# Optimization experiments

Hardware: AMD Instinct MI355X
Metric: run time of the kernel (lower is better)

Reference implementation:

```python
import jax, jax.numpy as jnp
import numpy as np

D, HID = 768, 192          # embed_dim, BiAttention hid_dim (= D//4)
B, LQ, NC, NE = 8, 64, 2048, 1200
NCON, NREL = 100000, 41    # concept vocab, relations (+1 pad)
SCALE = 0.02


def setup_inputs() -> dict:
    key = jax.random.key(0)
    ks = jax.random.split(key, 20)
    n = lambda k, s, sc=SCALE: jax.random.normal(k, s, jnp.float32) * sc
    return {
        'q_hidden_states': jax.random.normal(ks[0], (B, LQ, D), jnp.float32),
        'q_attention_mask': jnp.ones((B, LQ), jnp.bool_),
        'head_cids': jax.random.randint(ks[1], (B, NC), 0, NCON, jnp.int32),
        'distances': jax.random.randint(ks[2], (B, NC), 0, 4, jnp.int32),
        'head_idxs': jax.random.randint(ks[3], (B, NE), 0, NC, jnp.int32),
        'tail_idxs': jax.random.randint(ks[4], (B, NE), 0, NC, jnp.int32),
        'rel_ids': jax.random.randint(ks[5], (B, NE), 0, NREL, jnp.int32),
        'concept_table': n(ks[6], (NCON, D)),
        'dist_table': n(ks[7], (4, D)),
        'rel_table': n(ks[8], (NREL, D)),
        'W_ce': n(ks[9], (2 * D, D)), 'b_ce': jnp.zeros((D,), jnp.float32),
        'W_cs': n(ks[10], (D, 2 * D)), 'b_cs': jnp.zeros((2 * D,), jnp.float32),
        'W_ts': n(ks[11], (D, 5 * D)), 'b_ts': jnp.zeros((5 * D,), jnp.float32),
        'w_in1': n(ks[12], (D,)), 'w_mem1': n(ks[13], (D,)),
        'W_in2': n(ks[14], (D, HID)), 'b_in2': jnp.zeros((HID,), jnp.float32),
        'W_mem2': n(ks[15], (D, HID)), 'b_mem2': jnp.zeros((HID,), jnp.float32),
    }


def biattention(inp, mem, mask, w_in1, w_mem1, W_in2, b_in2, W_mem2, b_mem2):
    # inp: [B,Ld,D], mem: [B,Lm,D], mask: [B,Lm] float. Eval mode -> dropout off.
    input_dot = jnp.einsum('bnd,d->bn', inp, w_in1)[..., None]        # [B,Ld,1]
    memory_dot = jnp.einsum('bld,d->bl', mem, w_mem1)[:, None, :]     # [B,1,Lm]
    cross = jnp.einsum('bnd,bld->bnl', inp, mem) / np.sqrt(D)         # [B,Ld,Lm]
    att = input_dot + memory_dot + cross - 1e30 * (1.0 - mask[:, None, :])
    inp2 = inp @ W_in2 + b_in2                                        # [B,Ld,H]
    mem2 = mem @ W_mem2 + b_mem2                                      # [B,Lm,H]
    w1 = jax.nn.softmax(att, axis=-1)
    out1 = jnp.einsum('bnl,blh->bnh', w1, mem2)
    w2 = jax.nn.softmax(jnp.max(att, axis=-1), axis=-1)               # [B,Ld]
    out2 = jnp.einsum('bn,bnh->bh', w2, inp2)[:, None, :]             # [B,1,H]
    return jnp.concatenate([inp2, out1, inp2 * out1, out2 * out1], axis=-1)


def reference(q_hidden_states, q_attention_mask, head_cids, distances,
              head_idxs, tail_idxs, rel_ids, concept_table, dist_table,
              rel_table, W_ce, b_ce, W_cs, b_cs, W_ts, b_ts,
              w_in1, w_mem1, W_in2, b_in2, W_mem2, b_mem2):
    mask_f = q_attention_mask.astype(jnp.float32)
    # max-pooled question embedding (masked as in torch source)
    q_emb = jnp.max(q_hidden_states * mask_f[:, :, None], axis=1)     # [B,D]
    # concept encoding: gather concept + distance embeddings, fuse with linear
    c_emb = concept_table[head_cids]                                  # [B,NC,D]
    d_emb = dist_table[distances]                                     # [B,NC,D]
    cf = jnp.concatenate([c_emb, d_emb], axis=-1) @ W_ce + b_ce       # [B,NC,D]
    # BiAttention fusion of concepts against question tokens
    fused = biattention(cf, q_hidden_states, mask_f,
                        w_in1, w_mem1, W_in2, b_in2, W_mem2, b_mem2)  # [B,NC,D]
    # concept scoring: dot with concept_score_lin(q_emb) in 2D space
    c_query = q_emb @ W_cs + b_cs                                     # [B,2D]
    c_feats = jnp.concatenate([cf, fused], axis=-1)                   # [B,NC,2D]
    c_logits = jnp.einsum('bnd,bd->bn', c_feats, c_query)             # [B,NC]
    # triple scoring: gather head/tail concept features + relation embeddings
    h = jnp.take_along_axis(cf, head_idxs[..., None], axis=1)         # [B,NE,D]
    t = jnp.take_along_axis(cf, tail_idxs[..., None], axis=1)
    hf = jnp.take_along_axis(fused, head_idxs[..., None], axis=1)
    r = rel_table[rel_ids]                                            # [B,NE,D]
    t_feats = jnp.concatenate([h, r, t, h * t, hf], axis=-1)          # [B,NE,5D]
    t_query = q_emb @ W_ts + b_ts                                     # [B,5D]
    t_logits = jnp.einsum('bed,bd->be', t_feats, t_query)             # [B,NE]
    return jax.nn.sigmoid(jnp.concatenate([c_logits, t_logits], axis=-1))
```

## Files before the change

### kernel.cpp

```cpp
#include <hip/hip_runtime.h>
#include <hip/hip_bf16.h>
#include <math.h>

#define BD   768
#define HH   192
#define NB   8
#define NLQ  64
#define NNC  2048
#define NNE  1200
#define M_ROWS (NB*NNC)

typedef float  f32x4  __attribute__((ext_vector_type(4)));
typedef short  bf16x8 __attribute__((ext_vector_type(8)));

__device__ __forceinline__ float wave_sum64(float v){
  #pragma unroll
  for (int off = 32; off; off >>= 1) v += __shfl_xor(v, off);
  return v;
}
__device__ __forceinline__ unsigned short f2bf(float f){
  union { float f; unsigned int u; } v; v.f = f;
  unsigned int u = v.u + 0x7fffu + ((v.u >> 16) & 1u);
  return (unsigned short)(u >> 16);
}
__device__ __forceinline__ float bf2f(unsigned short h){
  union { unsigned int u; float f; } v; v.u = ((unsigned int)h) << 16; return v.f;
}
__device__ __forceinline__ unsigned int pack2(float lo, float hi){
  return ((unsigned int)f2bf(hi) << 16) | (unsigned int)f2bf(lo);
}

__global__ __launch_bounds__(256)
void k_wcvt(const float* __restrict__ W_ce, const float* __restrict__ W_in2,
            const float* __restrict__ qh, const float* __restrict__ w_in1,
            unsigned short* __restrict__ Wce_t, unsigned short* __restrict__ Win2_t,
            unsigned short* __restrict__ qhx){
  int idx = blockIdx.x * 256 + threadIdx.x;
  if (idx < 1179648) {
    int n = idx / 1536, k = idx - n * 1536;
    Wce_t[idx] = f2bf(W_ce[(size_t)k * BD + n]);
  } else if (idx < 1327104) {
    int i = idx - 1179648;
    int n = i / BD, k = i - n * BD;
    Win2_t[i] = f2bf(W_in2[(size_t)k * HH + n]);
  } else {
    int i = idx - 1327104;
    int b = i / 61440; int rk = i - b * 61440;
    int r = rk / BD, k = rk - r * BD;
    unsigned short v;
    if (r < 64)       v = f2bf(qh[((size_t)b * NLQ + r) * BD + k]);
    else if (r == 64) v = f2bf(w_in1[k] * 27.712812921102035f);
    else              v = 0;
    qhx[i] = v;
  }
}

__global__ __launch_bounds__(256)
void k_pre(const float* __restrict__ qh,
           const float* __restrict__ W_cs, const float* __restrict__ b_cs,
           const float* __restrict__ W_ts, const float* __restrict__ b_ts,
           const float* __restrict__ w_mem1,
           float* __restrict__ c_query, float* __restrict__ t_query,
           float* __restrict__ mdot){
  const int b = blockIdx.x, chunk = blockIdx.y, t = threadIdx.x;
  if (chunk == 21) {
    if (t < NLQ) {
      const float* q = qh + ((size_t)b * NLQ + t) * BD;
      float acc = 0.f;
      #pragma unroll 4
      for (int d = 0; d < BD; d += 4) {
        float4 v = *(const float4*)(q + d);
        acc += v.x*w_mem1[d] + v.y*w_mem1[d+1] + v.z*w_mem1[d+2] + v.w*w_mem1[d+3];
      }
      mdot[b * NLQ + t] = acc;
    }
    return;
  }
  __shared__ float qe[BD];
  for (int d = t; d < BD; d += 256) {
    const float* p = qh + (size_t)b * NLQ * BD + d;
    float m = -1e30f;
    for (int l = 0; l < NLQ; ++l) m = fmaxf(m, p[(size_t)l * BD]);
    qe[d] = m;
  }
  __syncthreads();
  int j = chunk * 256 + t;
  if (j < 1536) {
    float acc = b_cs[j];
    for (int d = 0; d < BD; ++d) acc += qe[d] * W_cs[(size_t)d * 1536 + j];
    c_query[b * 1536 + j] = acc;
  } else {
    int j2 = j - 1536;
    float acc = b_ts[j2];
    for (int d = 0; d < BD; ++d) acc += qe[d] * W_ts[(size_t)d * 3840 + j2];
    t_query[b * 3840 + j2] = acc;
  }
}

__global__ __launch_bounds__(256)
void k_cvt_gather(const int* __restrict__ cids, const int* __restrict__ dsts,
                  const float* __restrict__ ctab, const float* __restrict__ dtab,
                  unsigned short* __restrict__ Acat){
  int idx = blockIdx.x * 256 + threadIdx.x;
  int row = idx / 192, kc = (idx - row * 192) * 8;
  int cid = cids[row], dst = dsts[row];
  const float* src = (kc < BD) ? (ctab + (size_t)cid * BD + kc)
                               : (dtab + (size_t)dst * BD + (kc - BD));
  float4 f0 = ((const float4*)src)[0];
  float4 f1 = ((const float4*)src)[1];
  uint4 o;
  o.x = pack2(f0.x, f0.y); o.y = pack2(f0.z, f0.w);
  o.z = pack2(f1.x, f1.y); o.w = pack2(f1.z, f1.w);
  *(uint4*)(Acat + (size_t)row * 1536 + kc) = o;
}

__global__ void k_mem2(const float* __restrict__ qh, const float* __restrict__ W_mem2,
                       const float* __restrict__ b_mem2, float* __restrict__ mem2){
  int idx = blockIdx.x * blockDim.x + threadIdx.x;
  if (idx >= NB * NLQ * HH) return;
  int h = idx % HH; int bl = idx / HH;
  const float* q = qh + (size_t)bl * BD;
  float acc = b_mem2[h];
  for (int d = 0; d < BD; ++d) acc += q[d] * W_mem2[(size_t)d * HH + h];
  mem2[idx] = acc;
}

template<int BM, int BN, bool BF16OUT>
__global__ __launch_bounds__(256)
void gemm_bt(const unsigned short* __restrict__ A,
             const unsigned short* __restrict__ Bt,
             const float* __restrict__ bias,
             float* __restrict__ Cf, unsigned short* __restrict__ Cb,
             int K, int N)
{
  constexpr int BK = 32;
  __shared__ unsigned short As[BM * BK];
  __shared__ unsigned short Bs[BN * BK];
  const int tid = threadIdx.x;
  const int lane = tid & 63, wave = tid >> 6;
  const int m0 = blockIdx.x * BM, n0 = blockIdx.y * BN;
  const int wm = (wave & 1) * (BM / 2);
  const int wn = (wave >> 1) * (BN / 2);
  constexpr int FM = BM / 32, FN = BN / 32;
  constexpr int CA = (BM * 4) / 256, CB = (BN * 4) / 256;

  f32x4 acc[FM][FN] = {};
  const int fr = lane & 15;
  const int fk = (lane >> 4) * 8;

  for (int k0 = 0; k0 < K; k0 += BK) {
    __syncthreads();
    #pragma unroll
    for (int i = 0; i < CA; ++i) {
      int c = i * 256 + tid;
      const unsigned short* g = A + (size_t)(m0 + (c >> 2)) * K + k0 + (c & 3) * 8;
      __builtin_amdgcn_global_load_lds(
          (const __attribute__((address_space(1))) void*)g,
          (__attribute__((address_space(3))) void*)(As + c * 8), 16, 0, 0);
    }
    #pragma unroll
    for (int i = 0; i < CB; ++i) {
      int c = i * 256 + tid;
      const unsigned short* g = Bt + (size_t)(n0 + (c >> 2)) * K + k0 + (c & 3) * 8;
      __builtin_amdgcn_global_load_lds(
          (const __attribute__((address_space(1))) void*)g,
          (__attribute__((address_space(3))) void*)(Bs + c * 8), 16, 0, 0);
    }
    __syncthreads();
    bf16x8 af[FM], bfv[FN];
    #pragma unroll
    for (int mi = 0; mi < FM; ++mi)
      af[mi] = *(const bf16x8*)(As + (wm + mi * 16 + fr) * BK + fk);
    #pragma unroll
    for (int ni = 0; ni < FN; ++ni)
      bfv[ni] = *(const bf16x8*)(Bs + (wn + ni * 16 + fr) * BK + fk);
    #pragma unroll
    for (int mi = 0; mi < FM; ++mi)
      #pragma unroll
      for (int ni = 0; ni < FN; ++ni)
        acc[mi][ni] = __builtin_amdgcn_mfma_f32_16x16x32_bf16(
            af[mi], bfv[ni], acc[mi][ni], 0, 0, 0);
  }

  const int col16 = lane & 15, row4 = (lane >> 4) * 4;
  #pragma unroll
  for (int mi = 0; mi < FM; ++mi) {
    #pragma unroll
    for (int ni = 0; ni < FN; ++ni) {
      int col = n0 + wn + ni * 16 + col16;
      float bv = bias ? bias[col] : 0.0f;
      int rowb = m0 + wm + mi * 16 + row4;
      #pragma unroll
      for (int r = 0; r < 4; ++r) {
        float v = acc[mi][ni][r] + bv;
        size_t off = (size_t)(rowb + r) * N + col;
        if (BF16OUT) Cb[off] = f2bf(v);
        else         Cf[off] = v;
      }
    }
  }
}

__global__ __launch_bounds__(256)
void k_attf(const unsigned short* __restrict__ cf_bf,
            const unsigned short* __restrict__ qhx,
            const float* __restrict__ mdot,
            const float* __restrict__ mem2,
            float* __restrict__ out1, float* __restrict__ rowmax)
{
  __shared__ unsigned short As[64 * 32];
  __shared__ unsigned short Bs[80 * 32];
  __shared__ float Sbuf[64][81];
  const int tid = threadIdx.x, lane = tid & 63, wave = tid >> 6;
  const int m0 = blockIdx.x * 64, b = blockIdx.y;
  const unsigned short* Ab = cf_bf + ((size_t)b * NNC + m0) * BD;
  const unsigned short* Bb = qhx + (size_t)b * 80 * BD;
  const int fr = lane & 15, fk = (lane >> 4) * 8;
  const int wm = wave * 16;
  f32x4 acc[5] = {};

  for (int k0 = 0; k0 < BD; k0 += 32) {
    __syncthreads();
    {
      int c = tid;
      const unsigned short* g = Ab + (size_t)(c >> 2) * BD + k0 + (c & 3) * 8;
      __builtin_amdgcn_global_load_lds(
          (const __attribute__((address_space(1))) void*)g,
          (__attribute__((address_space(3))) void*)(As + c * 8), 16, 0, 0);
    }
    {
      int c = tid;
      const unsigned short* g = Bb + (size_t)(c >> 2) * BD + k0 + (c & 3) * 8;
      __builtin_amdgcn_global_load_lds(
          (const __attribute__((address_space(1))) void*)g,
          (__attribute__((address_space(3))) void*)(Bs + c * 8), 16, 0, 0);
      if (tid < 64) {
        c = 256 + tid;
        g = Bb + (size_t)(c >> 2) * BD + k0 + (c & 3) * 8;
        __builtin_amdgcn_global_load_lds(
            (const __attribute__((address_space(1))) void*)g,
            (__attribute__((address_space(3))) void*)(Bs + c * 8), 16, 0, 0);
      }
    }
    __syncthreads();
    bf16x8 af = *(const bf16x8*)(As + (wm + fr) * 32 + fk);
    #pragma unroll
    for (int ni = 0; ni < 5; ++ni) {
      bf16x8 bfv = *(const bf16x8*)(Bs + (ni * 16 + fr) * 32 + fk);
      acc[ni] = __builtin_amdgcn_mfma_f32_16x16x32_bf16(af, bfv, acc[ni], 0, 0, 0);
    }
  }
  __syncthreads();
  const int col16 = lane & 15, row4 = (lane >> 4) * 4;
  #pragma unroll
  for (int ni = 0; ni < 5; ++ni)
    #pragma unroll
    for (int r = 0; r < 4; ++r)
      Sbuf[wm + row4 + r][ni * 16 + col16] = acc[ni][r];
  __syncthreads();

  if (wave == 0) {
    const float scale = 0.03608439182435161f;
    const float* md = mdot + b * NLQ;
    const int r = lane;
    float m = -1e30f;
    for (int l = 0; l < NLQ; ++l)
      m = fmaxf(m, md[l] + Sbuf[r][l] * scale);
    rowmax[b * NNC + m0 + r] = m + Sbuf[r][64] * scale;
    float s = 0.f;
    for (int l = 0; l < NLQ; ++l) {
      float e = expf(md[l] + Sbuf[r][l] * scale - m);
      s += e;
      Sbuf[r][l] = e;
    }
    Sbuf[r][80] = 1.f / s;
  }
  __syncthreads();

  if (tid < HH) {
    const int h = tid;
    const float* m2 = mem2 + (size_t)b * NLQ * HH + h;
    #pragma unroll 1
    for (int r8 = 0; r8 < 8; ++r8) {
      float a[8] = {};
      for (int l = 0; l < NLQ; ++l) {
        float mv = m2[(size_t)l * HH];
        #pragma unroll
        for (int j = 0; j < 8; ++j) a[j] += Sbuf[r8 * 8 + j][l] * mv;
      }
      #pragma unroll
      for (int j = 0; j < 8; ++j) {
        int r = r8 * 8 + j;
        out1[((size_t)(b * NNC + m0 + r)) * HH + h] = a[j] * Sbuf[r][80];
      }
    }
  }
}

__global__ __launch_bounds__(256)
void k_w2(const float* __restrict__ rowmax, float* __restrict__ w2buf)
{
  const int b = blockIdx.x, t = threadIdx.x;
  __shared__ float red[256];
  const float* rm = rowmax + (size_t)b * NNC;
  float m = -1e30f;
  for (int n = t; n < NNC; n += 256) m = fmaxf(m, rm[n]);
  red[t] = m; __syncthreads();
  for (int s = 128; s; s >>= 1) { if (t < s) red[t] = fmaxf(red[t], red[t+s]); __syncthreads(); }
  m = red[0]; __syncthreads();
  float ssum = 0.f;
  for (int n = t; n < NNC; n += 256) { float e = expf(rm[n] - m); w2buf[b*NNC + n] = e; ssum += e; }
  red[t] = ssum; __syncthreads();
  for (int s = 128; s; s >>= 1) { if (t < s) red[t] += red[t+s]; __syncthreads(); }
  float inv = 1.f / red[0];
  for (int n = t; n < NNC; n += 256) w2buf[b*NNC + n] *= inv;
}

__global__ __launch_bounds__(192)
void k_out2p(const float* __restrict__ w2buf, const float* __restrict__ inp2,
             float* __restrict__ part)
{
  const int g = blockIdx.x, b = blockIdx.y, h = threadIdx.x;
  const float* w  = w2buf + (size_t)b * NNC + g * 128;
  const float* ip = inp2 + ((size_t)b * NNC + g * 128) * HH + h;
  float acc = 0.f;
  for (int n = 0; n < 128; ++n) acc += w[n] * ip[(size_t)n * HH];
  part[((size_t)b * 16 + g) * HH + h] = acc;
}
__global__ __launch_bounds__(192)
void k_out2r(const float* __restrict__ part, float* __restrict__ out2)
{
  const int b = blockIdx.x, h = threadIdx.x;
  float acc = 0.f;
  #pragma unroll
  for (int g = 0; g < 16; ++g) acc += part[((size_t)b * 16 + g) * HH + h];
  out2[b * HH + h] = acc;
}

__global__ __launch_bounds__(256)
void k_clogit(const unsigned short* __restrict__ cf_bf, const float* __restrict__ inp2,
              const float* __restrict__ out1, const float* __restrict__ out2,
              const float* __restrict__ c_query, float* __restrict__ out)
{
  const int bn = blockIdx.x * 4 + (threadIdx.x >> 6);
  const int b = bn >> 11, n = bn & 2047, lane = threadIdx.x & 63;
  const float* cq  = c_query + (size_t)b * 1536;
  const unsigned short* cfr = cf_bf + (size_t)bn * BD;
  const float* i2  = inp2 + (size_t)bn * HH;
  const float* o1  = out1 + (size_t)bn * HH;
  const float* o2  = out2 + (size_t)b * HH;
  float acc = 0.f;
  for (int d = lane; d < BD; d += 64) acc += bf2f(cfr[d]) * cq[d];
  #pragma unroll
  for (int j = 0; j < 3; ++j) {
    int h = lane + 64 * j;
    float a = i2[h], o = o1[h];
    acc += a * cq[768+h] + o * cq[960+h] + a*o * cq[1152+h] + o2[h]*o * cq[1344+h];
  }
  acc = wave_sum64(acc);
  if (lane == 0) out[(size_t)b * 3248 + n] = 1.f / (1.f + expf(-acc));
}

__global__ __launch_bounds__(256)
void k_tlogit(const unsigned short* __restrict__ cf_bf, const float* __restrict__ inp2,
              const float* __restrict__ out1, const float* __restrict__ out2,
              const float* __restrict__ t_query,
              const int* __restrict__ head_idxs, const int* __restrict__ tail_idxs,
              const int* __restrict__ rel_ids, const float* __restrict__ rtab,
              float* __restrict__ out)
{
  __shared__ float tqs[3840];
  const int b = blockIdx.x / 300;
  const int e = (blockIdx.x % 300) * 4 + (threadIdx.x >> 6);
  const int lane = threadIdx.x & 63;
  const float* tq = t_query + (size_t)b * 3840;
  for (int i = threadIdx.x; i < 3840; i += 256) tqs[i] = tq[i];
  __syncthreads();
  const int be = b * NNE + e;
  const int hi = head_idxs[be], ti = tail_idxs[be], rid = rel_ids[be];
  const unsigned short* ch = cf_bf + ((size_t)b * NNC + hi) * BD;
  const unsigned short* ct = cf_bf + ((size_t)b * NNC + ti) * BD;
  const float* rr = rtab + (size_t)rid * BD;
  const float* i2 = inp2 + ((size_t)b * NNC + hi) * HH;
  const float* o1 = out1 + ((size_t)b * NNC + hi) * HH;
  const float* o2 = out2 + (size_t)b * HH;
  float acc = 0.f;
  for (int d = lane; d < BD; d += 64) {
    float hd = bf2f(ch[d]), td = bf2f(ct[d]);
    acc += hd * tqs[d] + rr[d] * tqs[768+d] + td * tqs[1536+d] + hd*td * tqs[2304+d];
  }
  #pragma unroll
  for (int j = 0; j < 3; ++j) {
    int h = lane + 64 * j;
    float a = i2[h], o = o1[h];
    acc += a * tqs[3072+h] + o * tqs[3264+h] + a*o * tqs[3456+h] + o2[h]*o * tqs[3648+h];
  }
  acc = wave_sum64(acc);
  if (lane == 0) out[(size_t)b * 3248 + 2048 + e] = 1.f / (1.f + expf(-acc));
}

extern "C" void kernel_launch(void* const* d_in, const int* in_sizes, int n_in,
                              void* d_out, int out_size, void* d_ws, size_t ws_size,
                              hipStream_t stream) {
  const float* qh        = (const float*)d_in[0];
  const int*   head_cids = (const int*)d_in[2];
  const int*   distances = (const int*)d_in[3];
  const int*   head_idxs = (const int*)d_in[4];
  const int*   tail_idxs = (const int*)d_in[5];
  const int*   rel_ids   = (const int*)d_in[6];
  const float* ctab      = (const float*)d_in[7];
  const float* dtab      = (const float*)d_in[8];
  const float* rtab      = (const float*)d_in[9];
  const float* W_ce      = (const float*)d_in[10];
  const float* b_ce      = (const float*)d_in[11];
  const float* W_cs      = (const float*)d_in[12];
  const float* b_cs      = (const float*)d_in[13];
  const float* W_ts      = (const float*)d_in[14];
  const float* b_ts      = (const float*)d_in[15];
  const float* w_in1     = (const float*)d_in[16];
  const float* w_mem1    = (const float*)d_in[17];
  const float* W_in2     = (const float*)d_in[18];
  const float* b_in2     = (const float*)d_in[19];
  const float* W_mem2    = (const float*)d_in[20];
  const float* b_mem2    = (const float*)d_in[21];
  float* out = (float*)d_out;

  float* fp      = (float*)d_ws;
  float* c_query = fp;                    fp += 12288;
  float* t_query = fp;                    fp += 30720;
  float* mem2    = fp;                    fp += 98304;
  float* mdot    = fp;                    fp += 512;
  float* rowmax  = fp;                    fp += 16384;
  float* w2buf   = fp;                    fp += 16384;
  float* part    = fp;                    fp += 24576;
  float* out2    = fp;                    fp += 1536;
  float* inp2    = fp;                    fp += 3145728;
  float* out1    = fp;                    fp += 3145728;
  unsigned short* cf_bf  = (unsigned short*)fp;
  unsigned short* Wce_t  = cf_bf  + 12582912ull;
  unsigned short* Win2_t = Wce_t  + 1179648ull;
  unsigned short* qhx    = Win2_t + 147456ull;
  unsigned short* A_cat  = qhx    + 491520ull;

  k_cvt_gather<<<(M_ROWS*192)/256, 256, 0, stream>>>(head_cids, distances, ctab, dtab, A_cat);
  k_wcvt<<<7104, 256, 0, stream>>>(W_ce, W_in2, qh, w_in1, Wce_t, Win2_t, qhx);
  k_pre<<<dim3(NB, 22), 256, 0, stream>>>(qh, W_cs, b_cs, W_ts, b_ts, w_mem1,
                                          c_query, t_query, mdot);
  k_mem2<<<(NB*NLQ*HH)/256, 256, 0, stream>>>(qh, W_mem2, b_mem2, mem2);

  gemm_bt<128,128,true><<<dim3(M_ROWS/128, BD/128), 256, 0, stream>>>(
      A_cat, Wce_t, b_ce, nullptr, cf_bf, 1536, BD);
  gemm_bt<128,64,false><<<dim3(M_ROWS/128, HH/64), 256, 0, stream>>>(
      cf_bf, Win2_t, b_in2, inp2, nullptr, BD, HH);

  k_attf<<<dim3(NNC/64, NB), 256, 0, stream>>>(cf_bf, qhx, mdot, mem2, out1, rowmax);

  k_w2<<<NB, 256, 0, stream>>>(rowmax, w2buf);
  k_out2p<<<dim3(16, NB), 192, 0, stream>>>(w2buf, inp2, part);
  k_out2r<<<NB, 192, 0, stream>>>(part, out2);
  k_clogit<<<M_ROWS/4, 256, 0, stream>>>(cf_bf, inp2, out1, out2, c_query, out);
  k_tlogit<<<(NB*NNE)/4, 256, 0, stream>>>(cf_bf, inp2, out1, out2, t_query,
                                           head_idxs, tail_idxs, rel_ids, rtab, out);
}
```

Measured before the change: 688.6 us.

## Rework attention with MFMA out1, tiled transposes, and merged tail kernels

Replaces the strided weight-transpose conversion with shared-memory tiled transposes. The attention kernel now reads its operands directly from global memory instead of staging them in LDS, computes the softmax with all four waves, and computes out1 through bf16 MFMA against a transposed bf16 mem2. The w2/out2 path collapses into a single kernel per batch, and the concept and triple logit kernels merge into one launch. These changes target uncoalesced transpose traffic, the scalar out1 loop, and launch overhead. The cost is lower precision for w1 and mem2, and out2 is now computed by only 8 blocks.

After: 795.2 us. 1.15x slower.

```diff
diff --git a/kernel.cpp b/kernel.cpp
--- a/kernel.cpp
+++ b/kernel.cpp
@@ -31,28 +31,35 @@
 }
 
 __global__ __launch_bounds__(256)
-void k_wcvt(const float* __restrict__ W_ce, const float* __restrict__ W_in2,
-            const float* __restrict__ qh, const float* __restrict__ w_in1,
-            unsigned short* __restrict__ Wce_t, unsigned short* __restrict__ Win2_t,
-            unsigned short* __restrict__ qhx){
+void k_tcvt(const float* __restrict__ src, unsigned short* __restrict__ dst,
+            int R, int C){
+  __shared__ float T[32][33];
+  const int tx = threadIdx.x & 31, ty = threadIdx.x >> 5;
+  const int c0 = blockIdx.x * 32, r0 = blockIdx.y * 32;
+  #pragma unroll
+  for (int i = 0; i < 4; ++i)
+    T[ty + i * 8][tx] = src[(size_t)(r0 + ty + i * 8) * C + c0 + tx];
+  __syncthreads();
+  #pragma unroll
+  for (int i = 0; i < 4; ++i)
+    dst[(size_t)(c0 + ty + i * 8) * R + r0 + tx] = f2bf(T[tx][ty + i * 8]);
+}
+
+__global__ __launch_bounds__(256)
+void k_cvt_gather(const int* __restrict__ cids, const int* __restrict__ dsts,
+                  const float* __restrict__ ctab, const float* __restrict__ dtab,
+                  unsigned short* __restrict__ Acat){
   int idx = blockIdx.x * 256 + threadIdx.x;
-  if (idx < 1179648) {
-    int n = idx / 1536, k = idx - n * 1536;
-    Wce_t[idx] = f2bf(W_ce[(size_t)k * BD + n]);
-  } else if (idx < 1327104) {
-    int i = idx - 1179648;
-    int n = i / BD, k = i - n * BD;
-    Win2_t[i] = f2bf(W_in2[(size_t)k * HH + n]);
-  } else {
-    int i = idx - 1327104;
-    int b = i / 61440; int rk = i - b * 61440;
-    int r = rk / BD, k = rk - r * BD;
-    unsigned short v;
-    if (r < 64)       v = f2bf(qh[((size_t)b * NLQ + r) * BD + k]);
-    else if (r == 64) v = f2bf(w_in1[k] * 27.712812921102035f);
-    else              v = 0;
-    qhx[i] = v;
-  }
+  int row = idx / 192, kc = (idx - row * 192) * 8;
+  int cid = cids[row], dst = dsts[row];
+  const float* src = (kc < BD) ? (ctab + (size_t)cid * BD + kc)
+                               : (dtab + (size_t)dst * BD + (kc - BD));
+  float4 f0 = ((const float4*)src)[0];
+  float4 f1 = ((const float4*)src)[1];
+  uint4 o;
+  o.x = pack2(f0.x, f0.y); o.y = pack2(f0.z, f0.w);
+  o.z = pack2(f1.x, f1.y); o.w = pack2(f1.z, f1.w);
+  *(uint4*)(Acat + (size_t)row * 1536 + kc) = o;
 }
 
 __global__ __launch_bounds__(256)
@@ -98,31 +105,26 @@
 }
 
 __global__ __launch_bounds__(256)
-void k_cvt_gather(const int* __restrict__ cids, const int* __restrict__ dsts,
-                  const float* __restrict__ ctab, const float* __restrict__ dtab,
-                  unsigned short* __restrict__ Acat){
+void k_mem2qhx(const float* __restrict__ qh, const float* __restrict__ W_mem2,
+               const float* __restrict__ b_mem2, const float* __restrict__ w_in1,
+               unsigned short* __restrict__ mem2t, unsigned short* __restrict__ qhx){
   int idx = blockIdx.x * 256 + threadIdx.x;
-  int row = idx / 192, kc = (idx - row * 192) * 8;
-  int cid = cids[row], dst = dsts[row];
-  const float* src = (kc < BD) ? (ctab + (size_t)cid * BD + kc)
-                               : (dtab + (size_t)dst * BD + (kc - BD));
-  float4 f0 = ((const float4*)src)[0];
-  float4 f1 = ((const float4*)src)[1];
-  uint4 o;
-  o.x = pack2(f0.x, f0.y); o.y = pack2(f0.z, f0.w);
-  o.z = pack2(f1.x, f1.y); o.w = pack2(f1.z, f1.w);
-  *(uint4*)(Acat + (size_t)row * 1536 + kc) = o;
-}
-
-__global__ void k_mem2(const float* __restrict__ qh, const float* __restrict__ W_mem2,
-                       const float* __restrict__ b_mem2, float* __restrict__ mem2){
-  int idx = blockIdx.x * blockDim.x + threadIdx.x;
-  if (idx >= NB * NLQ * HH) return;
-  int h = idx % HH; int bl = idx / HH;
-  const float* q = qh + (size_t)bl * BD;
-  float acc = b_mem2[h];
-  for (int d = 0; d < BD; ++d) acc += q[d] * W_mem2[(size_t)d * HH + h];
-  mem2[idx] = acc;
+  if (idx < 98304) {
+    int l = idx & 63, h = (idx >> 6) % HH, b = idx / 12288;
+    const float* q = qh + ((size_t)b * NLQ + l) * BD;
+    float acc = b_mem2[h];
+    for (int d = 0; d < BD; ++d) acc += q[d] * W_mem2[(size_t)d * HH + h];
+    mem2t[((size_t)b * HH + h) * 64 + l] = f2bf(acc);
+  } else {
+    int i = idx - 98304;
+    int b = i / 61440, rk = i - b * 61440;
+    int r = rk / BD, k = rk - r * BD;
+    unsigned short v;
+    if (r < 64)       v = f2bf(qh[((size_t)b * NLQ + r) * BD + k]);
+    else if (r == 64) v = f2bf(w_in1[k] * 27.712812921102035f);
+    else              v = 0;
+    qhx[i] = v;
+  }
 }
 
 template<int BM, int BN, bool BF16OUT>
@@ -205,103 +207,89 @@
 void k_attf(const unsigned short* __restrict__ cf_bf,
             const unsigned short* __restrict__ qhx,
             const float* __restrict__ mdot,
-            const float* __restrict__ mem2,
+            const unsigned short* __restrict__ mem2t,
             float* __restrict__ out1, float* __restrict__ rowmax)
 {
-  __shared__ unsigned short As[64 * 32];
-  __shared__ unsigned short Bs[80 * 32];
   __shared__ float Sbuf[64][81];
+  __shared__ unsigned short w1buf[64][64];
+  __shared__ float mds[64];
   const int tid = threadIdx.x, lane = tid & 63, wave = tid >> 6;
   const int m0 = blockIdx.x * 64, b = blockIdx.y;
-  const unsigned short* Ab = cf_bf + ((size_t)b * NNC + m0) * BD;
+  if (tid < 64) mds[tid] = mdot[b * NLQ + tid];
+
+  const int fr = lane & 15, fk = (lane >> 4) * 8;
+  const unsigned short* Arow = cf_bf + ((size_t)(b * NNC + m0 + wave * 16 + fr)) * BD;
   const unsigned short* Bb = qhx + (size_t)b * 80 * BD;
-  const int fr = lane & 15, fk = (lane >> 4) * 8;
-  const int wm = wave * 16;
   f32x4 acc[5] = {};
-
+  #pragma unroll 2
   for (int k0 = 0; k0 < BD; k0 += 32) {
-    __syncthreads();
-    {
-      int c = tid;
-      const unsigned short* g = Ab + (size_t)(c >> 2) * BD + k0 + (c & 3) * 8;
-      __builtin_amdgcn_global_load_lds(
-          (const __attribute__((address_space(1))) void*)g,
-          (__attribute__((address_space(3))) void*)(As + c * 8), 16, 0, 0);
-    }
-    {
-      int c = tid;
-      const unsigned short* g = Bb + (size_t)(c >> 2) * BD + k0 + (c & 3) * 8;
-      __builtin_amdgcn_global_load_lds(
-          (const __attribute__((address_space(1))) void*)g,
-          (__attribute__((address_space(3))) void*)(Bs + c * 8), 16, 0, 0);
-      if (tid < 64) {
-        c = 256 + tid;
-        g = Bb + (size_t)(c >> 2) * BD + k0 + (c & 3) * 8;
-        __builtin_amdgcn_global_load_lds(
-            (const __attribute__((address_space(1))) void*)g,
-            (__attribute__((address_space(3))) void*)(Bs + c * 8), 16, 0, 0);
-      }
-    }
-    __syncthreads();
-    bf16x8 af = *(const bf16x8*)(As + (wm + fr) * 32 + fk);
+    bf16x8 af = *(const bf16x8*)(Arow + k0 + fk);
     #pragma unroll
     for (int ni = 0; ni < 5; ++ni) {
-      bf16x8 bfv = *(const bf16x8*)(Bs + (ni * 16 + fr) * 32 + fk);
-      acc[ni] = __builtin_amdgcn_mfma_f32_16x16x32_bf16(af, bfv, acc[ni], 0, 0, 0);
-    }
-  }
+      bf16x8 bv = *(const bf16x8*)(Bb + (size_t)(ni * 16 + fr) * BD + k0 + fk);
+      acc[ni] = __builtin_amdgcn_mfma_f32_16x16x32_bf16(af, bv, acc[ni], 0, 0, 0);
+    }
+  }
+  const int col16 = lane & 15, row4 = (lane >> 4) * 4;
+  #pragma unroll
+  for (int ni = 0; ni < 5; ++ni)
+    #pragma unroll
+    for (int r = 0; r < 4; ++r)
+      Sbuf[wave * 16 + row4 + r][ni * 16 + col16] = acc[ni][r];
   __syncthreads();
-  const int col16 = lane & 15, row4 = (lane >> 4) * 4;
-  #pragma unroll
-  for (int ni = 0; ni < 5; ++ni)
+
+  {
+    const float scale = 0.03608439182435161f;
+    const int r = wave * 16 + (lane >> 2);
+    const int q = lane & 3;
+    float e[16];
+    float mx = -1e30f;
+    #pragma unroll
+    for (int i = 0; i < 16; ++i) {
+      int l = q * 16 + i;
+      float v = mds[l] + Sbuf[r][l] * scale;
+      e[i] = v; mx = fmaxf(mx, v);
+    }
+    mx = fmaxf(mx, __shfl_xor(mx, 1));
+    mx = fmaxf(mx, __shfl_xor(mx, 2));
+    float s = 0.f;
+    #pragma unroll
+    for (int i = 0; i < 16; ++i) { e[i] = expf(e[i] - mx); s += e[i]; }
+    s += __shfl_xor(s, 1);
+    s += __shfl_xor(s, 2);
+    float inv = 1.f / s;
+    if (q == 0) rowmax[b * NNC + m0 + r] = mx + Sbuf[r][64] * scale;
+    #pragma unroll
+    for (int i = 0; i < 16; ++i) w1buf[r][q * 16 + i] = f2bf(e[i] * inv);
+  }
+  __syncthreads();
+
+  f32x4 acc2[12] = {};
+  const unsigned short* Mb = mem2t + (size_t)b * HH * 64;
+  #pragma unroll
+  for (int kk = 0; kk < 2; ++kk) {
+    bf16x8 af = *(const bf16x8*)(&w1buf[wave * 16 + fr][kk * 32 + fk]);
+    #pragma unroll
+    for (int ni = 0; ni < 12; ++ni) {
+      bf16x8 bv = *(const bf16x8*)(Mb + (size_t)(ni * 16 + fr) * 64 + kk * 32 + fk);
+      acc2[ni] = __builtin_amdgcn_mfma_f32_16x16x32_bf16(af, bv, acc2[ni], 0, 0, 0);
+    }
+  }
+  #pragma unroll
+  for (int ni = 0; ni < 12; ++ni)
     #pragma unroll
     for (int r = 0; r < 4; ++r)
-      Sbuf[wm + row4 + r][ni * 16 + col16] = acc[ni][r];
-  __syncthreads();
-
-  if (wave == 0) {
-    const float scale = 0.03608439182435161f;
-    const float* md = mdot + b * NLQ;
-    const int r = lane;
-    float m = -1e30f;
-    for (int l = 0; l < NLQ; ++l)
-      m = fmaxf(m, md[l] + Sbuf[r][l] * scale);
-    rowmax[b * NNC + m0 + r] = m + Sbuf[r][64] * scale;
-    float s = 0.f;
-    for (int l = 0; l < NLQ; ++l) {
-      float e = expf(md[l] + Sbuf[r][l] * scale - m);
-      s += e;
-      Sbuf[r][l] = e;
-    }
-    Sbuf[r][80] = 1.f / s;
-  }
-  __syncthreads();
-
-  if (tid < HH) {
-    const int h = tid;
-    const float* m2 = mem2 + (size_t)b * NLQ * HH + h;
-    #pragma unroll 1
-    for (int r8 = 0; r8 < 8; ++r8) {
-      float a[8] = {};
-      for (int l = 0; l < NLQ; ++l) {
-        float mv = m2[(size_t)l * HH];
-        #pragma unroll
-        for (int j = 0; j < 8; ++j) a[j] += Sbuf[r8 * 8 + j][l] * mv;
-      }
-      #pragma unroll
-      for (int j = 0; j < 8; ++j) {
-        int r = r8 * 8 + j;
-        out1[((size_t)(b * NNC + m0 + r)) * HH + h] = a[j] * Sbuf[r][80];
-      }
-    }
-  }
-}
-
-__global__ __launch_bounds__(256)
-void k_w2(const float* __restrict__ rowmax, float* __restrict__ w2buf)
+      out1[(size_t)(b * NNC + m0 + wave * 16 + row4 + r) * HH + ni * 16 + col16]
+          = acc2[ni][r];
+}
+
+__global__ __launch_bounds__(256)
+void k_w2out2(const float* __restrict__ rowmax, const float* __restrict__ inp2,
+              float* __restrict__ out2)
 {
   const int b = blockIdx.x, t = threadIdx.x;
   __shared__ float red[256];
+  __shared__ float w2s[NNC];
   const float* rm = rowmax + (size_t)b * NNC;
   float m = -1e30f;
   for (int n = t; n < NNC; n += 256) m = fmaxf(m, rm[n]);
@@ -309,94 +297,77 @@
   for (int s = 128; s; s >>= 1) { if (t < s) red[t] = fmaxf(red[t], red[t+s]); __syncthreads(); }
   m = red[0]; __syncthreads();
   float ssum = 0.f;
-  for (int n = t; n < NNC; n += 256) { float e = expf(rm[n] - m); w2buf[b*NNC + n] = e; ssum += e; }
+  for (int n = t; n < NNC; n += 256) { float e = expf(rm[n] - m); w2s[n] = e; ssum += e; }
   red[t] = ssum; __syncthreads();
   for (int s = 128; s; s >>= 1) { if (t < s) red[t] += red[t+s]; __syncthreads(); }
   float inv = 1.f / red[0];
-  for (int n = t; n < NNC; n += 256) w2buf[b*NNC + n] *= inv;
-}
-
-__global__ __launch_bounds__(192)
-void k_out2p(const float* __restrict__ w2buf, const float* __restrict__ inp2,
-             float* __restrict__ part)
-{
-  const int g = blockIdx.x, b = blockIdx.y, h = threadIdx.x;
-  const float* w  = w2buf + (size_t)b * NNC + g * 128;
-  const float* ip = inp2 + ((size_t)b * NNC + g * 128) * HH + h;
-  float acc = 0.f;
-  for (int n = 0; n < 128; ++n) acc += w[n] * ip[(size_t)n * HH];
-  part[((size_t)b * 16 + g) * HH + h] = acc;
-}
-__global__ __launch_bounds__(192)
-void k_out2r(const float* __restrict__ part, float* __restrict__ out2)
-{
-  const int b = blockIdx.x, h = threadIdx.x;
-  float acc = 0.f;
-  #pragma unroll
-  for (int g = 0; g < 16; ++g) acc += part[((size_t)b * 16 + g) * HH + h];
-  out2[b * HH + h] = acc;
-}
-
-__global__ __launch_bounds__(256)
-void k_clogit(const unsigned short* __restrict__ cf_bf, const float* __restrict__ inp2,
+  __syncthreads();
+  if (t < HH) {
+    float acc = 0.f;
+    const float* ip = inp2 + (size_t)b * NNC * HH + t;
+    #pragma unroll 4
+    for (int n = 0; n < NNC; ++n) acc += w2s[n] * ip[(size_t)n * HH];
+    out2[b * HH + t] = acc * inv;
+  }
+}
+
+__global__ __launch_bounds__(256)
+void k_logits(const unsigned short* __restrict__ cf_bf, const float* __restrict__ inp2,
               const float* __restrict__ out1, const float* __restrict__ out2,
-              const float* __restrict__ c_query, float* __restrict__ out)
-{
-  const int bn = blockIdx.x * 4 + (threadIdx.x >> 6);
-  const int b = bn >> 11, n = bn & 2047, lane = threadIdx.x & 63;
-  const float* cq  = c_query + (size_t)b * 1536;
-  const unsigned short* cfr = cf_bf + (size_t)bn * BD;
-  const float* i2  = inp2 + (size_t)bn * HH;
-  const float* o1  = out1 + (size_t)bn * HH;
-  const float* o2  = out2 + (size_t)b * HH;
-  float acc = 0.f;
-  for (int d = lane; d < BD; d += 64) acc += bf2f(cfr[d]) * cq[d];
-  #pragma unroll
-  for (int j = 0; j < 3; ++j) {
-    int h = lane + 64 * j;
-    float a = i2[h], o = o1[h];
-    acc += a * cq[768+h] + o * cq[960+h] + a*o * cq[1152+h] + o2[h]*o * cq[1344+h];
-  }
-  acc = wave_sum64(acc);
-  if (lane == 0) out[(size_t)b * 3248 + n] = 1.f / (1.f + expf(-acc));
-}
-
-__global__ __launch_bounds__(256)
-void k_tlogit(const unsigned short* __restrict__ cf_bf, const float* __restrict__ inp2,
-              const float* __restrict__ out1, const float* __restrict__ out2,
-              const float* __restrict__ t_query,
+              const float* __restrict__ c_query, const float* __restrict__ t_query,
               const int* __restrict__ head_idxs, const int* __restrict__ tail_idxs,
               const int* __restrict__ rel_ids, const float* __restrict__ rtab,
               float* __restrict__ out)
 {
   __shared__ float tqs[3840];
-  const int b = blockIdx.x / 300;
-  const int e = (blockIdx.x % 300) * 4 + (threadIdx.x >> 6);
-  const int lane = threadIdx.x & 63;
-  const float* tq = t_query + (size_t)b * 3840;
-  for (int i = threadIdx.x; i < 3840; i += 256) tqs[i] = tq[i];
-  __syncthreads();
-  const int be = b * NNE + e;
-  const int hi = head_idxs[be], ti = tail_idxs[be], rid = rel_ids[be];
-  const unsigned short* ch = cf_bf + ((size_t)b * NNC + hi) * BD;
-  const unsigned short* ct = cf_bf + ((size_t)b * NNC + ti) * BD;
-  const float* rr = rtab + (size_t)rid * BD;
-  const float* i2 = inp2 + ((size_t)b * NNC + hi) * HH;
-  const float* o1 = out1 + ((size_t)b * NNC + hi) * HH;
-  const float* o2 = out2 + (size_t)b * HH;
-  float acc = 0.f;
-  for (int d = lane; d < BD; d += 64) {
-    float hd = bf2f(ch[d]), td = bf2f(ct[d]);
-    acc += hd * tqs[d] + rr[d] * tqs[768+d] + td * tqs[1536+d] + hd*td * tqs[2304+d];
-  }
-  #pragma unroll
-  for (int j = 0; j < 3; ++j) {
-    int h = lane + 64 * j;
-    float a = i2[h], o = o1[h];
-    acc += a * tqs[3072+h] + o * tqs[3264+h] + a*o * tqs[3456+h] + o2[h]*o * tqs[3648+h];
-  }
-  acc = wave_sum64(acc);
-  if (lane == 0) out[(size_t)b * 3248 + 2048 + e] = 1.f / (1.f + expf(-acc));
+  const int blk = blockIdx.x, lane = threadIdx.x & 63, w = threadIdx.x >> 6;
+  if (blk < 4096) {
+    const int bn = blk * 4 + w;
+    const int b = bn >> 11, n = bn & 2047;
+    const float* cq  = c_query + (size_t)b * 1536;
+    const unsigned short* cfr = cf_bf + (size_t)bn * BD;
+    const float* i2  = inp2 + (size_t)bn * HH;
+    const float* o1  = out1 + (size_t)bn * HH;
+    const float* o2  = out2 + (size_t)b * HH;
+    float acc = 0.f;
+    for (int d = lane; d < BD; d += 64) acc += bf2f(cfr[d]) * cq[d];
+    #pragma unroll
+    for (int j = 0; j < 3; ++j) {
+      int h = lane + 64 * j;
+      float a = i2[h], o = o1[h];
+      acc += a * cq[768+h] + o * cq[960+h] + a*o * cq[1152+h] + o2[h]*o * cq[1344+h];
+    }
+    acc = wave_sum64(acc);
+    if (lane == 0) out[(size_t)b * 3248 + n] = 1.f / (1.f + expf(-acc));
+  } else {
+    const int blk2 = blk - 4096;
+    const int b = blk2 / 300;
+    const int e = (blk2 % 300) * 4 + w;
+    const float* tq = t_query + (size_t)b * 3840;
+    for (int i = threadIdx.x; i < 3840; i += 256) tqs[i] = tq[i];
+    __syncthreads();
+    const int be = b * NNE + e;
+    const int hi = head_idxs[be], ti = tail_idxs[be], rid = rel_ids[be];
+    const unsigned short* ch = cf_bf + ((size_t)b * NNC + hi) * BD;
+    const unsigned short* ct = cf_bf + ((size_t)b * NNC + ti) * BD;
+    const float* rr = rtab + (size_t)rid * BD;
+    const float* i2 = inp2 + ((size_t)b * NNC + hi) * HH;
+    const float* o1 = out1 + ((size_t)b * NNC + hi) * HH;
+    const float* o2 = out2 + (size_t)b * HH;
+    float acc = 0.f;
+    for (int d = lane; d < BD; d += 64) {
+      float hd = bf2f(ch[d]), td = bf2f(ct[d]);
+      acc += hd * tqs[d] + rr[d] * tqs[768+d] + td * tqs[1536+d] + hd*td * tqs[2304+d];
+    }
+    #pragma unroll
+    for (int j = 0; j < 3; ++j) {
+      int h = lane + 64 * j;
+      float a = i2[h], o = o1[h];
+      acc += a * tqs[3072+h] + o * tqs[3264+h] + a*o * tqs[3456+h] + o2[h]*o * tqs[3648+h];
+    }
+    acc = wave_sum64(acc);
+    if (lane == 0) out[(size_t)b * 3248 + 2048 + e] = 1.f / (1.f + expf(-acc));
+  }
 }
 
 extern "C" void kernel_launch(void* const* d_in, const int* in_sizes, int n_in,
@@ -428,11 +399,8 @@
   float* fp      = (float*)d_ws;
   float* c_query = fp;                    fp += 12288;
   float* t_query = fp;                    fp += 30720;
-  float* mem2    = fp;                    fp += 98304;
   float* mdot    = fp;                    fp += 512;
   float* rowmax  = fp;                    fp += 16384;
-  float* w2buf   = fp;                    fp += 16384;
-  float* part    = fp;                    fp += 24576;
   float* out2    = fp;                    fp += 1536;
   float* inp2    = fp;                    fp += 3145728;
   float* out1    = fp;                    fp += 3145728;
@@ -440,25 +408,25 @@
   unsigned short* Wce_t  = cf_bf  + 12582912ull;
   unsigned short* Win2_t = Wce_t  + 1179648ull;
   unsigned short* qhx    = Win2_t + 147456ull;
-  unsigned short* A_cat  = qhx    + 491520ull;
-
+  unsigned short* mem2t  = qhx    + 491520ull;
+  unsigned short* A_cat  = mem2t  + 98304ull;
+
+  k_tcvt<<<dim3(BD/32, 1536/32), 256, 0, stream>>>(W_ce, Wce_t, 1536, BD);
+  k_tcvt<<<dim3(HH/32, BD/32), 256, 0, stream>>>(W_in2, Win2_t, BD, HH);
   k_cvt_gather<<<(M_ROWS*192)/256, 256, 0, stream>>>(head_cids, distances, ctab, dtab, A_cat);
-  k_wcvt<<<7104, 256, 0, stream>>>(W_ce, W_in2, qh, w_in1, Wce_t, Win2_t, qhx);
   k_pre<<<dim3(NB, 22), 256, 0, stream>>>(qh, W_cs, b_cs, W_ts, b_ts, w_mem1,
                                           c_query, t_query, mdot);
-  k_mem2<<<(NB*NLQ*HH)/256, 256, 0, stream>>>(qh, W_mem2, b_mem2, mem2);
+  k_mem2qhx<<<(98304 + 491520)/256, 256, 0, stream>>>(qh, W_mem2, b_mem2, w_in1,
+                                                      mem2t, qhx);
 
   gemm_bt<128,128,true><<<dim3(M_ROWS/128, BD/128), 256, 0, stream>>>(
       A_cat, Wce_t, b_ce, nullptr, cf_bf, 1536, BD);
   gemm_bt<128,64,false><<<dim3(M_ROWS/128, HH/64), 256, 0, stream>>>(
       cf_bf, Win2_t, b_in2, inp2, nullptr, BD, HH);
 
-  k_attf<<<dim3(NNC/64, NB), 256, 0, stream>>>(cf_bf, qhx, mdot, mem2, out1, rowmax);
-
-  k_w2<<<NB, 256, 0, stream>>>(rowmax, w2buf);
-  k_out2p<<<dim3(16, NB), 192, 0, stream>>>(w2buf, inp2, part);
-  k_out2r<<<NB, 192, 0, stream>>>(part, out2);
-  k_clogit<<<M_ROWS/4, 256, 0, stream>>>(cf_bf, inp2, out1, out2, c_query, out);
-  k_tlogit<<<(NB*NNE)/4, 256, 0, stream>>>(cf_bf, inp2, out1, out2, t_query,
-                                           head_idxs, tail_idxs, rel_ids, rtab, out);
-}
+  k_attf<<<dim3(NNC/64, NB), 256, 0, stream>>>(cf_bf, qhx, mdot, mem2t, out1, rowmax);
+
+  k_w2out2<<<NB, 256, 0, stream>>>(rowmax, inp2, out2);
+  k_logits<<<4096 + 2400, 256, 0, stream>>>(cf_bf, inp2, out1, out2, c_query, t_query,
+                                            head_idxs, tail_idxs, rel_ids, rtab, out);
+}
```
